# Optimization experiments

Measured on AMD Instinct MI355X. Metric: run time of the kernel, lower is better.

The kernel has to match this reference:

```python
import jax, jax.numpy as jnp
import numpy as np

LN_EPS = 1e-5


def _gather(x, idx):
    # x: [B, N, C], idx: [B, N, K] -> [B, N, K, C]
    return jax.vmap(lambda xb, ib: xb[ib])(x, idx)


def setup_inputs() -> dict:
    key = jax.random.key(0)
    ks = jax.random.split(key, 8)
    B, N, K, C_in, C_out, GEO = 2, 16384, 32, 128, 128, 10
    return {
        "points": jax.random.normal(ks[0], (B, N, 3), dtype=jnp.float32),
        "features": jax.random.normal(ks[1], (B, N, C_in), dtype=jnp.float32),
        "grouped_idx": jax.random.randint(ks[2], (B, N, K), 0, N, dtype=jnp.int32),
        "w_pos": jax.random.normal(ks[3], (GEO, C_in), dtype=jnp.float32) * (GEO ** -0.5),
        "b_pos": jnp.zeros((C_in,), jnp.float32),
        "w_gcm": jax.random.normal(ks[4], (C_in, C_in), dtype=jnp.float32) * (C_in ** -0.5),
        "b_gcm": jnp.zeros((C_in,), jnp.float32),
        "w_out": jax.random.normal(ks[5], (C_in, C_out), dtype=jnp.float32) * (C_in ** -0.5),
        "b_out": jnp.zeros((C_out,), jnp.float32),
        "ln_g": jnp.ones((C_out,), jnp.float32),
        "ln_b": jnp.zeros((C_out,), jnp.float32),
    }


def reference(points, features, grouped_idx, w_pos, b_pos, w_gcm, b_gcm,
              w_out, b_out, ln_g, ln_b):
    # gather neighbor coords and features: [B, N, K, *]
    grouped_pts = _gather(points, grouped_idx)
    xyz = points[..., 0:3]                      # [B, N, 3]
    grouped_xyz = grouped_pts[..., 0:3]         # [B, N, K, 3]
    center = xyz[:, :, None, :]                 # [B, N, 1, 3]
    diff = grouped_xyz - center                 # xi - xj
    dist = jnp.linalg.norm(diff, axis=-1, keepdims=True)  # ||xi - xj||
    K = grouped_xyz.shape[2]
    geo = jnp.concatenate(
        [jnp.broadcast_to(center, grouped_xyz.shape), grouped_xyz, diff, dist],
        axis=-1)                                # [B, N, K, 10]
    expanded_f = geo @ w_pos + b_pos            # pos_proj -> [B, N, K, C_in]
    grouped_f = _gather(features, grouped_idx)  # [B, N, K, C_in]
    h = jax.nn.relu((grouped_f + expanded_f) @ w_gcm + b_gcm)  # gcm_layer
    pooled = jnp.max(h, axis=2)                 # maxpooling over neighbors
    res = pooled + features                     # residual
    o = res @ w_out + b_out                     # out Linear
    mu = jnp.mean(o, axis=-1, keepdims=True)
    var = jnp.mean((o - mu) ** 2, axis=-1, keepdims=True)
    o = (o - mu) * jax.lax.rsqrt(var + LN_EPS) * ln_g + ln_b  # LayerNorm
    return jax.nn.relu(o)
```

## Files before the change

kernel.cpp:

```cpp
#include <hip/hip_runtime.h>
#include <hip/hip_bf16.h>
#include <math.h>

typedef __attribute__((ext_vector_type(8))) short short8;
typedef __attribute__((ext_vector_type(4))) short short4v;
typedef __attribute__((ext_vector_type(4))) float float4v;
typedef unsigned short ushort_t;

constexpr int NPTS = 32768;
constexpr int NN   = 16384;
constexpr int KK   = 32;
constexpr int CC   = 128;
constexpr int GRP  = 16;
constexpr int SG   = 40;
constexpr int SR   = 136;
#define LN_EPS 1e-5f

constexpr size_t WS_WP   = 0;
constexpr size_t WS_WO   = 40960;
constexpr size_t WS_BE   = 73728;
constexpr size_t WS_PG   = 74240;
constexpr size_t WS_FB   = 79360;
constexpr size_t WS_NEED = WS_FB + (size_t)NPTS * CC * 2;

__device__ __forceinline__ short f2bs(float x) {
    return (short)__builtin_bit_cast(unsigned short, __float2bfloat16(x));
}
__device__ __forceinline__ float bs2f(ushort_t u) {
    return __uint_as_float(((unsigned)u) << 16);
}

__global__ __launch_bounds__(128) void prep_fold(
    const float* __restrict__ w_pos, const float* __restrict__ b_pos,
    const float* __restrict__ w_gcm, const float* __restrict__ b_gcm,
    float* __restrict__ wsPG, float* __restrict__ wsBeff)
{
    const int c = threadIdx.x, g = blockIdx.x;
    if (g < 10) {
        float s = 0.f;
        #pragma unroll
        for (int r = 0; r < 128; ++r) s += w_pos[g * 128 + r] * w_gcm[r * 128 + c];
        wsPG[g * 128 + c] = s;
    } else {
        float s = b_gcm[c];
        #pragma unroll
        for (int r = 0; r < 128; ++r) s += b_pos[r] * w_gcm[r * 128 + c];
        wsBeff[c] = s;
    }
}

__global__ __launch_bounds__(256) void prep_pack(
    const float* __restrict__ features, const float* __restrict__ w_gcm,
    const float* __restrict__ w_out, const float* __restrict__ wsPG,
    short* __restrict__ wsWp, short* __restrict__ wsWo, ushort_t* __restrict__ featbf,
    int do_convert)
{
    const int t = threadIdx.x, blk = blockIdx.x;
    if (blk < 512) {
        if (!do_convert) return;
        const int base = blk * 2048 + t;
        #pragma unroll
        for (int i = 0; i < 8; ++i) {
            const int f4 = base + i * 256;
            const float4 a = ((const float4*)features)[f4];
            short4v v; v[0]=f2bs(a.x); v[1]=f2bs(a.y); v[2]=f2bs(a.z); v[3]=f2bs(a.w);
            ((short4v*)featbf)[f4] = v;
        }
        return;
    }
    if (blk == 512) {
        #pragma unroll 4
        for (int e = t; e < 16 * 128 * 8; e += 256) {
            const int j = e & 7, n = (e >> 3) & 127, g = e >> 10;
            wsWp[e] = f2bs(w_gcm[(g * 8 + j) * 128 + n]);
        }
        return;
    }
    if (blk == 513) {
        #pragma unroll 4
        for (int e2 = t; e2 < 4 * 128 * 8; e2 += 256) {
            const int e = 16 * 128 * 8 + e2;
            const int j = e & 7, n = (e >> 3) & 127, g = e >> 10;
            const int k = g * 8 + j;
            wsWp[e] = (k < 138) ? f2bs(wsPG[(k - 128) * 128 + n]) : (short)0;
        }
        return;
    }
    #pragma unroll 4
    for (int e = t; e < 128 * 128; e += 256) {
        const int j = e & 7, n = (e >> 3) & 127, g = e >> 10;
        wsWo[e] = f2bs(w_out[(g * 8 + j) * 128 + n]);
    }
}

template<int DMA>
__global__ __launch_bounds__(256) void bridge_main(
    const float* __restrict__ points, const float* __restrict__ features,
    const int*   __restrict__ gidx,
    const short* __restrict__ wsWp, const short* __restrict__ wsWo,
    const float* __restrict__ wsBeff, const ushort_t* __restrict__ featbf,
    const float* __restrict__ b_out, const float* __restrict__ ln_g,
    const float* __restrict__ ln_b,
    float* __restrict__ out)
{
    __shared__ short sA[2][KK * CC];
    __shared__ short sG[2][KK * SG];
    __shared__ short sRes[GRP * SR];
    __shared__ int   sIdx[GRP * KK];
    __shared__ float sPS[4][GRP], sPQ[4][GRP];

    const int t = threadIdx.x, wv = t >> 6, lane = t & 63;
    const int quad = (t >> 4) & 3, m = t & 15;
    const int g0 = blockIdx.x * GRP;
    const int nbase = (g0 >= NN) ? NN : 0;
    const int col0 = wv * 32 + m;

    sIdx[t]       = gidx[(size_t)g0 * KK + t];
    sIdx[t + 256] = gidx[(size_t)g0 * KK + t + 256];
    if (t < 128) {
        const int b = t >> 6, r = (t >> 1) & 31, h = t & 1;
        *(short8*)&sG[b][r * SG + 16 + h * 8] = (short8)0;
    }

    short8 bWp[5][2];
    #pragma unroll
    for (int ks = 0; ks < 5; ++ks)
        #pragma unroll
        for (int ntl = 0; ntl < 2; ++ntl)
            bWp[ks][ntl] = *((const short8*)wsWp + ((ks * 4 + quad) * 128 + col0 + ntl * 16));
    float beffv[2] = { wsBeff[col0], wsBeff[col0 + 16] };

    __syncthreads();

    const int r0 = wv * 4 + (lane >> 4);
    const int pc = lane & 15;
    const int gc = pc ^ r0;

    float4 ff0a, ff0b, ff1a, ff1b;
    float gcx, gcy, gcz, ggx, ggy, ggz;

    auto issue_dma = [&](int p, int buf) {
        const int kn0 = nbase + sIdx[p * KK + r0];
        const int kn1 = nbase + sIdx[p * KK + r0 + 16];
        const ushort_t* gp0 = featbf + (size_t)kn0 * CC + gc * 8;
        const ushort_t* gp1 = featbf + (size_t)kn1 * CC + gc * 8;
        short* l0 = &sA[buf][(wv * 4) * CC];
        short* l1 = &sA[buf][(wv * 4 + 16) * CC];
        __builtin_amdgcn_global_load_lds((const __attribute__((address_space(1))) void*)gp0,
                                         (__attribute__((address_space(3))) void*)l0, 16, 0, 0);
        __builtin_amdgcn_global_load_lds((const __attribute__((address_space(1))) void*)gp1,
                                         (__attribute__((address_space(3))) void*)l1, 16, 0, 0);
    };
    auto fb_load = [&](int p) {
        const int kn0 = nbase + sIdx[p * KK + r0];
        const int kn1 = nbase + sIdx[p * KK + r0 + 16];
        const float4* f0 = (const float4*)(features + (size_t)kn0 * CC + gc * 8);
        const float4* f1 = (const float4*)(features + (size_t)kn1 * CC + gc * 8);
        ff0a = f0[0]; ff0b = f0[1]; ff1a = f1[0]; ff1b = f1[1];
    };
    auto fb_store = [&](int buf) {
        short8 v;
        v[0]=f2bs(ff0a.x); v[1]=f2bs(ff0a.y); v[2]=f2bs(ff0a.z); v[3]=f2bs(ff0a.w);
        v[4]=f2bs(ff0b.x); v[5]=f2bs(ff0b.y); v[6]=f2bs(ff0b.z); v[7]=f2bs(ff0b.w);
        *(short8*)&sA[buf][r0 * CC + pc * 8] = v;
        v[0]=f2bs(ff1a.x); v[1]=f2bs(ff1a.y); v[2]=f2bs(ff1a.z); v[3]=f2bs(ff1a.w);
        v[4]=f2bs(ff1b.x); v[5]=f2bs(ff1b.y); v[6]=f2bs(ff1b.z); v[7]=f2bs(ff1b.w);
        *(short8*)&sA[buf][(r0 + 16) * CC + pc * 8] = v;
    };
    auto geo_load = [&](int p) {
        if (lane < 8) {
            const int j  = wv * 8 + lane;
            const int pt = g0 + p;
            const int kn = nbase + sIdx[p * KK + j];
            gcx = points[(size_t)pt * 3 + 0]; gcy = points[(size_t)pt * 3 + 1]; gcz = points[(size_t)pt * 3 + 2];
            ggx = points[(size_t)kn * 3 + 0]; ggy = points[(size_t)kn * 3 + 1]; ggz = points[(size_t)kn * 3 + 2];
        }
    };
    auto geo_store = [&](int buf) {
        if (lane < 8) {
            const int j = wv * 8 + lane;
            const float dx = ggx - gcx, dy = ggy - gcy, dz = ggz - gcz;
            const float dist = sqrtf(dx * dx + dy * dy + dz * dz);
            short8 v0, v1 = (short8)0;
            v0[0]=f2bs(gcx); v0[1]=f2bs(gcy); v0[2]=f2bs(gcz);
            v0[3]=f2bs(ggx); v0[4]=f2bs(ggy); v0[5]=f2bs(ggz);
            v0[6]=f2bs(dx);  v0[7]=f2bs(dy);
            v1[0]=f2bs(dz);  v1[1]=f2bs(dist);
            *(short8*)&sG[buf][j * SG + 0] = v0;
            *(short8*)&sG[buf][j * SG + 8] = v1;
        }
    };

    if constexpr (DMA) issue_dma(0, 0); else fb_load(0);
    geo_load(0);
    if constexpr (!DMA) fb_store(0);
    geo_store(0);
    __syncthreads();

    int offA[4];
    #pragma unroll
    for (int ks = 0; ks < 4; ++ks) offA[ks] = m * CC + (((ks * 4 + quad) ^ m) * 8);
    const int offG = m * SG + quad * 8;

    for (int p = 0; p < GRP; ++p) {
        const int buf = p & 1, nbuf = buf ^ 1;
        if (p + 1 < GRP) {
            if constexpr (DMA) issue_dma(p + 1, nbuf); else fb_load(p + 1);
            geo_load(p + 1);
        }

        const short* ab = sA[buf];
        const short* ag = sG[buf];
        float4v acc[2][2] = {};
        #pragma unroll
        for (int ks = 0; ks < 4; ++ks) {
            const short8 a0 = *(const short8*)(ab + offA[ks]);
            const short8 a1 = *(const short8*)(ab + offA[ks] + 16 * CC);
            acc[0][0] = __builtin_amdgcn_mfma_f32_16x16x32_bf16(a0, bWp[ks][0], acc[0][0], 0, 0, 0);
            acc[0][1] = __builtin_amdgcn_mfma_f32_16x16x32_bf16(a0, bWp[ks][1], acc[0][1], 0, 0, 0);
            acc[1][0] = __builtin_amdgcn_mfma_f32_16x16x32_bf16(a1, bWp[ks][0], acc[1][0], 0, 0, 0);
            acc[1][1] = __builtin_amdgcn_mfma_f32_16x16x32_bf16(a1, bWp[ks][1], acc[1][1], 0, 0, 0);
        }
        {
            const short8 a0 = *(const short8*)(ag + offG);
            const short8 a1 = *(const short8*)(ag + offG + 16 * SG);
            acc[0][0] = __builtin_amdgcn_mfma_f32_16x16x32_bf16(a0, bWp[4][0], acc[0][0], 0, 0, 0);
            acc[0][1] = __builtin_amdgcn_mfma_f32_16x16x32_bf16(a0, bWp[4][1], acc[0][1], 0, 0, 0);
            acc[1][0] = __builtin_amdgcn_mfma_f32_16x16x32_bf16(a1, bWp[4][0], acc[1][0], 0, 0, 0);
            acc[1][1] = __builtin_amdgcn_mfma_f32_16x16x32_bf16(a1, bWp[4][1], acc[1][1], 0, 0, 0);
        }

        if (p + 1 < GRP) {
            if constexpr (!DMA) fb_store(nbuf);
            geo_store(nbuf);
        }

        const int pt = g0 + p;
        #pragma unroll
        for (int ntl = 0; ntl < 2; ++ntl) {
            float v = acc[0][ntl][0];
            #pragma unroll
            for (int r = 1; r < 4; ++r) v = fmaxf(v, acc[0][ntl][r]);
            #pragma unroll
            for (int r = 0; r < 4; ++r) v = fmaxf(v, acc[1][ntl][r]);
            v = fmaxf(v, __shfl_xor(v, 16));
            v = fmaxf(v, __shfl_xor(v, 32));
            v = fmaxf(v + beffv[ntl], 0.f);
            float fc;
            if constexpr (DMA) fc = bs2f(featbf[(size_t)pt * CC + col0 + ntl * 16]);
            else               fc = features[(size_t)pt * CC + col0 + ntl * 16];
            const float res = v + fc;
            if (quad == 0) sRes[p * SR + col0 + ntl * 16] = f2bs(res);
        }
        __syncthreads();
    }

    short8 bWo[4][2];
    #pragma unroll
    for (int ks = 0; ks < 4; ++ks)
        #pragma unroll
        for (int ntl = 0; ntl < 2; ++ntl)
            bWo[ks][ntl] = *((const short8*)wsWo + ((ks * 4 + quad) * 128 + col0 + ntl * 16));

    const short* rm = sRes + m * SR;
    float4v acc2[2] = {};
    #pragma unroll
    for (int ks = 0; ks < 4; ++ks) {
        const short8 a = *(const short8*)(rm + ks * 32 + quad * 8);
        acc2[0] = __builtin_amdgcn_mfma_f32_16x16x32_bf16(a, bWo[ks][0], acc2[0], 0, 0, 0);
        acc2[1] = __builtin_amdgcn_mfma_f32_16x16x32_bf16(a, bWo[ks][1], acc2[1], 0, 0, 0);
    }

    const float boutv[2] = { b_out[col0], b_out[col0 + 16] };
    const float lngv[2]  = { ln_g[col0], ln_g[col0 + 16] };
    const float lnbv[2]  = { ln_b[col0], ln_b[col0 + 16] };

    #pragma unroll
    for (int r = 0; r < 4; ++r) {
        const float o0 = acc2[0][r] + boutv[0];
        const float o1 = acc2[1][r] + boutv[1];
        float ss = o0 + o1, qq = o0 * o0 + o1 * o1;
        #pragma unroll
        for (int d = 1; d < 16; d <<= 1) { ss += __shfl_xor(ss, d); qq += __shfl_xor(qq, d); }
        if (m == 0) { sPS[wv][quad * 4 + r] = ss; sPQ[wv][quad * 4 + r] = qq; }
    }
    __syncthreads();

    #pragma unroll
    for (int r = 0; r < 4; ++r) {
        const int R = quad * 4 + r;
        const float S = sPS[0][R] + sPS[1][R] + sPS[2][R] + sPS[3][R];
        const float Q = sPQ[0][R] + sPQ[1][R] + sPQ[2][R] + sPQ[3][R];
        const float mu  = S * (1.f / 128.f);
        const float var = fmaxf(Q * (1.f / 128.f) - mu * mu, 0.f);
        const float rstd = rsqrtf(var + LN_EPS);
        const float o0 = acc2[0][r] + boutv[0];
        const float o1 = acc2[1][r] + boutv[1];
        const size_t base = (size_t)(g0 + R) * CC;
        out[base + col0]      = fmaxf((o0 - mu) * rstd * lngv[0] + lnbv[0], 0.f);
        out[base + col0 + 16] = fmaxf((o1 - mu) * rstd * lngv[1] + lnbv[1], 0.f);
    }
}

extern "C" void kernel_launch(void* const* d_in, const int* in_sizes, int n_in,
                              void* d_out, int out_size, void* d_ws, size_t ws_size,
                              hipStream_t stream) {
    const float* points   = (const float*)d_in[0];
    const float* features = (const float*)d_in[1];
    const int*   gidx     = (const int*)  d_in[2];
    const float* w_pos    = (const float*)d_in[3];
    const float* b_pos    = (const float*)d_in[4];
    const float* w_gcm    = (const float*)d_in[5];
    const float* b_gcm    = (const float*)d_in[6];
    const float* w_out    = (const float*)d_in[7];
    const float* b_out    = (const float*)d_in[8];
    const float* ln_g     = (const float*)d_in[9];
    const float* ln_b     = (const float*)d_in[10];
    float* out = (float*)d_out;

    char* ws = (char*)d_ws;
    short*    wsWp   = (short*)(ws + WS_WP);
    short*    wsWo   = (short*)(ws + WS_WO);
    float*    wsBeff = (float*)(ws + WS_BE);
    float*    wsPG   = (float*)(ws + WS_PG);
    ushort_t* featbf = (ushort_t*)(ws + WS_FB);

    const bool use_dma = (ws_size >= WS_NEED);

    hipLaunchKernelGGL(prep_fold, dim3(11), dim3(128), 0, stream,
                       w_pos, b_pos, w_gcm, b_gcm, wsPG, wsBeff);
    hipLaunchKernelGGL(prep_pack, dim3(515), dim3(256), 0, stream,
                       features, w_gcm, w_out, wsPG, wsWp, wsWo, featbf,
                       use_dma ? 1 : 0);
    if (use_dma) {
        hipLaunchKernelGGL((bridge_main<1>), dim3(NPTS / GRP), dim3(256), 0, stream,
                           points, features, gidx, wsWp, wsWo, wsBeff, featbf,
                           b_out, ln_g, ln_b, out);
    } else {
        hipLaunchKernelGGL((bridge_main<0>), dim3(NPTS / GRP), dim3(256), 0, stream,
                           points, features, gidx, wsWp, wsWo, wsBeff, featbf,
                           b_out, ln_g, ln_b, out);
    }
}
```

Baseline: 163.1 us.

## Load gathered neighbor features directly into MFMA register fragments, drop LDS staging

Replaces the LDS double-buffer (global_load_lds DMA into shared tiles, then LDS reads for MFMA) with direct per-lane global loads of bf16 feature fragments into registers, double-buffered across the point loop. Geometry features are now computed in registers inside the MFMA A-fragment instead of being staged in LDS, and the per-point __syncthreads is removed by fully unrolling the loop with register prefetch. This removes LDS traffic and barriers, but raises register pressure (two buffers of fragments) and loses the swizzled coalesced access pattern, which may reduce occupancy or memory efficiency.

```diff
diff --git a/kernel.cpp b/kernel.cpp
--- a/kernel.cpp
+++ b/kernel.cpp
@@ -12,9 +12,9 @@
 constexpr int KK   = 32;
 constexpr int CC   = 128;
 constexpr int GRP  = 16;
-constexpr int SG   = 40;
 constexpr int SR   = 136;
 #define LN_EPS 1e-5f
+#define MFMA   __builtin_amdgcn_mfma_f32_16x16x32_bf16
 
 constexpr size_t WS_WP   = 0;
 constexpr size_t WS_WO   = 40960;
@@ -93,7 +93,7 @@
     }
 }
 
-template<int DMA>
+template<int FB>
 __global__ __launch_bounds__(256) void bridge_main(
     const float* __restrict__ points, const float* __restrict__ features,
     const int*   __restrict__ gidx,
@@ -103,24 +103,18 @@
     const float* __restrict__ ln_b,
     float* __restrict__ out)
 {
-    __shared__ short sA[2][KK * CC];
-    __shared__ short sG[2][KK * SG];
+    __shared__ int   sIdx[GRP * KK];
     __shared__ short sRes[GRP * SR];
-    __shared__ int   sIdx[GRP * KK];
     __shared__ float sPS[4][GRP], sPQ[4][GRP];
 
     const int t = threadIdx.x, wv = t >> 6, lane = t & 63;
-    const int quad = (t >> 4) & 3, m = t & 15;
+    const int quad = (lane >> 4) & 3, m = lane & 15;
     const int g0 = blockIdx.x * GRP;
     const int nbase = (g0 >= NN) ? NN : 0;
     const int col0 = wv * 32 + m;
 
     sIdx[t]       = gidx[(size_t)g0 * KK + t];
     sIdx[t + 256] = gidx[(size_t)g0 * KK + t + 256];
-    if (t < 128) {
-        const int b = t >> 6, r = (t >> 1) & 31, h = t & 1;
-        *(short8*)&sG[b][r * SG + 16 + h * 8] = (short8)0;
-    }
 
     short8 bWp[5][2];
     #pragma unroll
@@ -128,132 +122,132 @@
         #pragma unroll
         for (int ntl = 0; ntl < 2; ++ntl)
             bWp[ks][ntl] = *((const short8*)wsWp + ((ks * 4 + quad) * 128 + col0 + ntl * 16));
-    float beffv[2] = { wsBeff[col0], wsBeff[col0 + 16] };
+    const float beffv[2] = { wsBeff[col0], wsBeff[col0 + 16] };
 
     __syncthreads();
 
-    const int r0 = wv * 4 + (lane >> 4);
-    const int pc = lane & 15;
-    const int gc = pc ^ r0;
-
-    float4 ff0a, ff0b, ff1a, ff1b;
-    float gcx, gcy, gcz, ggx, ggy, ggz;
-
-    auto issue_dma = [&](int p, int buf) {
-        const int kn0 = nbase + sIdx[p * KK + r0];
-        const int kn1 = nbase + sIdx[p * KK + r0 + 16];
-        const ushort_t* gp0 = featbf + (size_t)kn0 * CC + gc * 8;
-        const ushort_t* gp1 = featbf + (size_t)kn1 * CC + gc * 8;
-        short* l0 = &sA[buf][(wv * 4) * CC];
-        short* l1 = &sA[buf][(wv * 4 + 16) * CC];
-        __builtin_amdgcn_global_load_lds((const __attribute__((address_space(1))) void*)gp0,
-                                         (__attribute__((address_space(3))) void*)l0, 16, 0, 0);
-        __builtin_amdgcn_global_load_lds((const __attribute__((address_space(1))) void*)gp1,
-                                         (__attribute__((address_space(3))) void*)l1, 16, 0, 0);
+    int      kn[2][2];
+    short8   fA[2][4][2];
+    float    geoR[2][9];
+    ushort_t residU[2][2];
+    float    residF[2][2];
+
+    auto ldIdx = [&](int p, int buf) {
+        kn[buf][0] = nbase + sIdx[p * KK + m];
+        kn[buf][1] = nbase + sIdx[p * KK + 16 + m];
     };
-    auto fb_load = [&](int p) {
-        const int kn0 = nbase + sIdx[p * KK + r0];
-        const int kn1 = nbase + sIdx[p * KK + r0 + 16];
-        const float4* f0 = (const float4*)(features + (size_t)kn0 * CC + gc * 8);
-        const float4* f1 = (const float4*)(features + (size_t)kn1 * CC + gc * 8);
-        ff0a = f0[0]; ff0b = f0[1]; ff1a = f1[0]; ff1b = f1[1];
+
+    auto ldFrag = [&](int p, int buf) {
+        const int pt = g0 + p;
+        if constexpr (FB) {
+            const short8* b0 = (const short8*)(featbf + (size_t)kn[buf][0] * CC);
+            const short8* b1 = (const short8*)(featbf + (size_t)kn[buf][1] * CC);
+            #pragma unroll
+            for (int ks = 0; ks < 4; ++ks) {
+                fA[buf][ks][0] = b0[ks * 4 + quad];
+                fA[buf][ks][1] = b1[ks * 4 + quad];
+            }
+            if (quad == 0) {
+                residU[buf][0] = featbf[(size_t)pt * CC + col0];
+                residU[buf][1] = featbf[(size_t)pt * CC + col0 + 16];
+            }
+        } else {
+            const float4* c0 = (const float4*)(features + (size_t)kn[buf][0] * CC);
+            const float4* c1 = (const float4*)(features + (size_t)kn[buf][1] * CC);
+            #pragma unroll
+            for (int ks = 0; ks < 4; ++ks) {
+                const float4 x0 = c0[ks * 8 + quad * 2], x1 = c0[ks * 8 + quad * 2 + 1];
+                const float4 y0 = c1[ks * 8 + quad * 2], y1 = c1[ks * 8 + quad * 2 + 1];
+                short8 v;
+                v[0]=f2bs(x0.x); v[1]=f2bs(x0.y); v[2]=f2bs(x0.z); v[3]=f2bs(x0.w);
+                v[4]=f2bs(x1.x); v[5]=f2bs(x1.y); v[6]=f2bs(x1.z); v[7]=f2bs(x1.w);
+                fA[buf][ks][0] = v;
+                v[0]=f2bs(y0.x); v[1]=f2bs(y0.y); v[2]=f2bs(y0.z); v[3]=f2bs(y0.w);
+                v[4]=f2bs(y1.x); v[5]=f2bs(y1.y); v[6]=f2bs(y1.z); v[7]=f2bs(y1.w);
+                fA[buf][ks][1] = v;
+            }
+            if (quad == 0) {
+                residF[buf][0] = features[(size_t)pt * CC + col0];
+                residF[buf][1] = features[(size_t)pt * CC + col0 + 16];
+            }
+        }
+        if (quad < 2) {
+            const float* pc = points + (size_t)pt * 3;
+            const float* p0 = points + (size_t)kn[buf][0] * 3;
+            const float* p1 = points + (size_t)kn[buf][1] * 3;
+            geoR[buf][0] = pc[0]; geoR[buf][1] = pc[1]; geoR[buf][2] = pc[2];
+            geoR[buf][3] = p0[0]; geoR[buf][4] = p0[1]; geoR[buf][5] = p0[2];
+            geoR[buf][6] = p1[0]; geoR[buf][7] = p1[1]; geoR[buf][8] = p1[2];
+        }
     };
-    auto fb_store = [&](int buf) {
-        short8 v;
-        v[0]=f2bs(ff0a.x); v[1]=f2bs(ff0a.y); v[2]=f2bs(ff0a.z); v[3]=f2bs(ff0a.w);
-        v[4]=f2bs(ff0b.x); v[5]=f2bs(ff0b.y); v[6]=f2bs(ff0b.z); v[7]=f2bs(ff0b.w);
-        *(short8*)&sA[buf][r0 * CC + pc * 8] = v;
-        v[0]=f2bs(ff1a.x); v[1]=f2bs(ff1a.y); v[2]=f2bs(ff1a.z); v[3]=f2bs(ff1a.w);
-        v[4]=f2bs(ff1b.x); v[5]=f2bs(ff1b.y); v[6]=f2bs(ff1b.z); v[7]=f2bs(ff1b.w);
-        *(short8*)&sA[buf][(r0 + 16) * CC + pc * 8] = v;
-    };
-    auto geo_load = [&](int p) {
-        if (lane < 8) {
-            const int j  = wv * 8 + lane;
-            const int pt = g0 + p;
-            const int kn = nbase + sIdx[p * KK + j];
-            gcx = points[(size_t)pt * 3 + 0]; gcy = points[(size_t)pt * 3 + 1]; gcz = points[(size_t)pt * 3 + 2];
-            ggx = points[(size_t)kn * 3 + 0]; ggy = points[(size_t)kn * 3 + 1]; ggz = points[(size_t)kn * 3 + 2];
-        }
-    };
-    auto geo_store = [&](int buf) {
-        if (lane < 8) {
-            const int j = wv * 8 + lane;
-            const float dx = ggx - gcx, dy = ggy - gcy, dz = ggz - gcz;
-            const float dist = sqrtf(dx * dx + dy * dy + dz * dz);
-            short8 v0, v1 = (short8)0;
-            v0[0]=f2bs(gcx); v0[1]=f2bs(gcy); v0[2]=f2bs(gcz);
-            v0[3]=f2bs(ggx); v0[4]=f2bs(ggy); v0[5]=f2bs(ggz);
-            v0[6]=f2bs(dx);  v0[7]=f2bs(dy);
-            v1[0]=f2bs(dz);  v1[1]=f2bs(dist);
-            *(short8*)&sG[buf][j * SG + 0] = v0;
-            *(short8*)&sG[buf][j * SG + 8] = v1;
-        }
-    };
-
-    if constexpr (DMA) issue_dma(0, 0); else fb_load(0);
-    geo_load(0);
-    if constexpr (!DMA) fb_store(0);
-    geo_store(0);
-    __syncthreads();
-
-    int offA[4];
-    #pragma unroll
-    for (int ks = 0; ks < 4; ++ks) offA[ks] = m * CC + (((ks * 4 + quad) ^ m) * 8);
-    const int offG = m * SG + quad * 8;
-
-    for (int p = 0; p < GRP; ++p) {
-        const int buf = p & 1, nbuf = buf ^ 1;
-        if (p + 1 < GRP) {
-            if constexpr (DMA) issue_dma(p + 1, nbuf); else fb_load(p + 1);
-            geo_load(p + 1);
-        }
-
-        const short* ab = sA[buf];
-        const short* ag = sG[buf];
+
+    auto compute = [&](int p, int buf) {
         float4v acc[2][2] = {};
         #pragma unroll
         for (int ks = 0; ks < 4; ++ks) {
-            const short8 a0 = *(const short8*)(ab + offA[ks]);
-            const short8 a1 = *(const short8*)(ab + offA[ks] + 16 * CC);
-            acc[0][0] = __builtin_amdgcn_mfma_f32_16x16x32_bf16(a0, bWp[ks][0], acc[0][0], 0, 0, 0);
-            acc[0][1] = __builtin_amdgcn_mfma_f32_16x16x32_bf16(a0, bWp[ks][1], acc[0][1], 0, 0, 0);
-            acc[1][0] = __builtin_amdgcn_mfma_f32_16x16x32_bf16(a1, bWp[ks][0], acc[1][0], 0, 0, 0);
-            acc[1][1] = __builtin_amdgcn_mfma_f32_16x16x32_bf16(a1, bWp[ks][1], acc[1][1], 0, 0, 0);
-        }
-        {
-            const short8 a0 = *(const short8*)(ag + offG);
-            const short8 a1 = *(const short8*)(ag + offG + 16 * SG);
-            acc[0][0] = __builtin_amdgcn_mfma_f32_16x16x32_bf16(a0, bWp[4][0], acc[0][0], 0, 0, 0);
-            acc[0][1] = __builtin_amdgcn_mfma_f32_16x16x32_bf16(a0, bWp[4][1], acc[0][1], 0, 0, 0);
-            acc[1][0] = __builtin_amdgcn_mfma_f32_16x16x32_bf16(a1, bWp[4][0], acc[1][0], 0, 0, 0);
-            acc[1][1] = __builtin_amdgcn_mfma_f32_16x16x32_bf16(a1, bWp[4][1], acc[1][1], 0, 0, 0);
-        }
-
-        if (p + 1 < GRP) {
-            if constexpr (!DMA) fb_store(nbuf);
-            geo_store(nbuf);
-        }
-
-        const int pt = g0 + p;
+            acc[0][0] = MFMA(fA[buf][ks][0], bWp[ks][0], acc[0][0], 0, 0, 0);
+            acc[0][1] = MFMA(fA[buf][ks][0], bWp[ks][1], acc[0][1], 0, 0, 0);
+            acc[1][0] = MFMA(fA[buf][ks][1], bWp[ks][0], acc[1][0], 0, 0, 0);
+            acc[1][1] = MFMA(fA[buf][ks][1], bWp[ks][1], acc[1][1], 0, 0, 0);
+        }
+        short8 ga0 = (short8)0, ga1 = (short8)0;
+        if (quad < 2) {
+            const float cx  = geoR[buf][0], cy  = geoR[buf][1], cz  = geoR[buf][2];
+            const float axx = geoR[buf][3], ayy = geoR[buf][4], azz = geoR[buf][5];
+            const float bxx = geoR[buf][6], byy = geoR[buf][7], bzz = geoR[buf][8];
+            const float d0x = axx - cx, d0y = ayy - cy, d0z = azz - cz;
+            const float d1x = bxx - cx, d1y = byy - cy, d1z = bzz - cz;
+            const float ds0 = sqrtf(d0x * d0x + d0y * d0y + d0z * d0z);
+            const float ds1 = sqrtf(d1x * d1x + d1y * d1y + d1z * d1z);
+            if (quad == 0) {
+                ga0[0]=f2bs(cx);  ga0[1]=f2bs(cy);  ga0[2]=f2bs(cz);
+                ga0[3]=f2bs(axx); ga0[4]=f2bs(ayy); ga0[5]=f2bs(azz);
+                ga0[6]=f2bs(d0x); ga0[7]=f2bs(d0y);
+                ga1[0]=f2bs(cx);  ga1[1]=f2bs(cy);  ga1[2]=f2bs(cz);
+                ga1[3]=f2bs(bxx); ga1[4]=f2bs(byy); ga1[5]=f2bs(bzz);
+                ga1[6]=f2bs(d1x); ga1[7]=f2bs(d1y);
+            } else {
+                ga0[0]=f2bs(d0z); ga0[1]=f2bs(ds0);
+                ga1[0]=f2bs(d1z); ga1[1]=f2bs(ds1);
+            }
+        }
+        acc[0][0] = MFMA(ga0, bWp[4][0], acc[0][0], 0, 0, 0);
+        acc[0][1] = MFMA(ga0, bWp[4][1], acc[0][1], 0, 0, 0);
+        acc[1][0] = MFMA(ga1, bWp[4][0], acc[1][0], 0, 0, 0);
+        acc[1][1] = MFMA(ga1, bWp[4][1], acc[1][1], 0, 0, 0);
+
         #pragma unroll
         for (int ntl = 0; ntl < 2; ++ntl) {
             float v = acc[0][ntl][0];
             #pragma unroll
-            for (int r = 1; r < 4; ++r) v = fmaxf(v, acc[0][ntl][r]);
+            for (int rr = 1; rr < 4; ++rr) v = fmaxf(v, acc[0][ntl][rr]);
             #pragma unroll
-            for (int r = 0; r < 4; ++r) v = fmaxf(v, acc[1][ntl][r]);
+            for (int rr = 0; rr < 4; ++rr) v = fmaxf(v, acc[1][ntl][rr]);
             v = fmaxf(v, __shfl_xor(v, 16));
             v = fmaxf(v, __shfl_xor(v, 32));
             v = fmaxf(v + beffv[ntl], 0.f);
-            float fc;
-            if constexpr (DMA) fc = bs2f(featbf[(size_t)pt * CC + col0 + ntl * 16]);
-            else               fc = features[(size_t)pt * CC + col0 + ntl * 16];
-            const float res = v + fc;
-            if (quad == 0) sRes[p * SR + col0 + ntl * 16] = f2bs(res);
-        }
-        __syncthreads();
-    }
+            if (quad == 0) {
+                float fc;
+                if constexpr (FB) fc = bs2f(residU[buf][ntl]);
+                else              fc = residF[buf][ntl];
+                sRes[p * SR + col0 + ntl * 16] = f2bs(v + fc);
+            }
+        }
+    };
+
+    ldIdx(0, 0);
+    ldFrag(0, 0);
+    ldIdx(1, 1);
+
+    #pragma unroll
+    for (int p = 0; p < GRP; ++p) {
+        const int buf = p & 1;
+        if (p + 1 < GRP) ldFrag(p + 1, buf ^ 1);
+        if (p + 2 < GRP) ldIdx(p + 2, buf);
+        compute(p, buf);
+    }
+
+    __syncthreads();
 
     short8 bWo[4][2];
     #pragma unroll
@@ -267,8 +261,8 @@
     #pragma unroll
     for (int ks = 0; ks < 4; ++ks) {
         const short8 a = *(const short8*)(rm + ks * 32 + quad * 8);
-        acc2[0] = __builtin_amdgcn_mfma_f32_16x16x32_bf16(a, bWo[ks][0], acc2[0], 0, 0, 0);
-        acc2[1] = __builtin_amdgcn_mfma_f32_16x16x32_bf16(a, bWo[ks][1], acc2[1], 0, 0, 0);
+        acc2[0] = MFMA(a, bWo[ks][0], acc2[0], 0, 0, 0);
+        acc2[1] = MFMA(a, bWo[ks][1], acc2[1], 0, 0, 0);
     }
 
     const float boutv[2] = { b_out[col0], b_out[col0 + 16] };
@@ -325,14 +319,14 @@
     float*    wsPG   = (float*)(ws + WS_PG);
     ushort_t* featbf = (ushort_t*)(ws + WS_FB);
 
-    const bool use_dma = (ws_size >= WS_NEED);
+    const bool use_bf = (ws_size >= WS_NEED);
 
     hipLaunchKernelGGL(prep_fold, dim3(11), dim3(128), 0, stream,
                        w_pos, b_pos, w_gcm, b_gcm, wsPG, wsBeff);
     hipLaunchKernelGGL(prep_pack, dim3(515), dim3(256), 0, stream,
                        features, w_gcm, w_out, wsPG, wsWp, wsWo, featbf,
-                       use_dma ? 1 : 0);
-    if (use_dma) {
+                       use_bf ? 1 : 0);
+    if (use_bf) {
         hipLaunchKernelGGL((bridge_main<1>), dim3(NPTS / GRP), dim3(256), 0, stream,
                            points, features, gidx, wsWp, wsWo, wsBeff, featbf,
                            b_out, ln_g, ln_b, out);
```

Result: slower. 231.6 us (+41.9%).
